# Kernel optimization log

Measured on AMD Instinct MI355X. Metric: run time of the kernel, lower is better.

The kernel has to match this reference:

```python
import jax, jax.numpy as jnp
import numpy as np

M, IN, OUT = 32, 4096, 16384

def setup_inputs() -> dict:
    key = jax.random.key(0)
    k1, k2, k3 = jax.random.split(key, 3)
    x = jax.random.normal(k1, (M, IN), dtype=jnp.float32)
    weight_q = jax.random.randint(k2, (OUT, IN), 0, 256, dtype=jnp.int32)  # uint8 codes
    bias = jax.random.normal(k3, (OUT,), dtype=jnp.float32)
    return {"x": x, "weight_q": weight_q, "zero": 128, "scale": jnp.float32(0.01), "bias": bias}

def reference(x, weight_q, zero, scale, bias):
    # Dequantize: w = scale * (q - zero), per-tensor affine
    w = scale * (weight_q.astype(jnp.float32) - jnp.float32(zero))  # [OUT, IN]
    # F.linear: y = x @ w.T + b
    return jnp.einsum('mi,oi->mo', x, w) + bias
```

## Files before the change

kernel.cpp:

```cpp
#include <hip/hip_runtime.h>

#define M_DIM 32
#define K_DIM 4096
#define N_DIM 16384
#define BN 16
#define BK 128
#define NSTAGE 32
#define LROW 136

using short8 = __attribute__((ext_vector_type(8))) short;
using f32x4  = __attribute__((ext_vector_type(4))) float;

__device__ __forceinline__ ushort f2bf_rne(float f) {
    unsigned u = __float_as_uint(f);
    u += 0x7fffu + ((u >> 16) & 1u);
    return (ushort)(u >> 16);
}

__device__ __forceinline__ ushort i2bf_exact(int v) {
    return (ushort)(__float_as_uint((float)v) >> 16);
}

__device__ __forceinline__ ushort4 cvt4(int4 v, int zero) {
    ushort4 o;
    o.x = i2bf_exact(v.x - zero);
    o.y = i2bf_exact(v.y - zero);
    o.z = i2bf_exact(v.z - zero);
    o.w = i2bf_exact(v.w - zero);
    return o;
}

__global__ __launch_bounds__(256) void prep_x_kernel(const float* __restrict__ x,
                                                     ushort* __restrict__ xb) {
    int i = blockIdx.x * blockDim.x + threadIdx.x;
    float4 v = reinterpret_cast<const float4*>(x)[i];
    ushort4 o;
    o.x = f2bf_rne(v.x); o.y = f2bf_rne(v.y); o.z = f2bf_rne(v.z); o.w = f2bf_rne(v.w);
    reinterpret_cast<ushort4*>(xb)[i] = o;
}

__global__ __launch_bounds__(256) void qgemm_kernel(
        const ushort* __restrict__ xb, const int* __restrict__ wq,
        const int* __restrict__ zerop, const float* __restrict__ scalep,
        const float* __restrict__ bias, float* __restrict__ out) {
    __shared__ ushort tile[BN][LROW];
    __shared__ float  red[4][M_DIM][BN];

    const int tid  = threadIdx.x;
    const int wave = tid >> 6;
    const int lane = tid & 63;
    const int quad = lane >> 4;
    const int l16  = lane & 15;
    const int n0   = blockIdx.x * BN;
    const int zero = *zerop;
    const int phase = blockIdx.x & (NSTAGE - 1);

    const int srow0 = wave * 4 + (lane >> 5);
    const int srow1 = srow0 + 2;
    const int sofs  = (lane & 31) * 4;
    const int* gb0 = wq + (size_t)(n0 + srow0) * K_DIM + sofs;
    const int* gb1 = wq + (size_t)(n0 + srow1) * K_DIM + sofs;

    const int bofs = wave * 32 + quad * 8;
    const ushort* axp0 = xb + (size_t)l16 * K_DIM + bofs;
    const ushort* axp1 = axp0 + 16 * K_DIM;

    f32x4 acc0 = {0.f, 0.f, 0.f, 0.f};
    f32x4 acc1 = {0.f, 0.f, 0.f, 0.f};

    int4 c0 = *(const int4*)(gb0 + phase * BK);
    int4 c1 = *(const int4*)(gb1 + phase * BK);

    #pragma unroll 1
    for (int s = 0; s < NSTAGE; ++s) {
        int4 nx0, nx1;
        if (s + 1 < NSTAGE) {
            int sn = ((s + 1 + phase) & (NSTAGE - 1)) * BK;
            nx0 = *(const int4*)(gb0 + sn);
            nx1 = *(const int4*)(gb1 + sn);
        }
        __syncthreads();
        *(ushort4*)&tile[srow0][sofs] = cvt4(c0, zero);
        *(ushort4*)&tile[srow1][sofs] = cvt4(c1, zero);
        __syncthreads();

        const int k0 = ((s + phase) & (NSTAGE - 1)) * BK;
        short8 a0 = *(const short8*)(axp0 + k0);
        short8 a1 = *(const short8*)(axp1 + k0);
        short8 bf = *(const short8*)&tile[l16][bofs];
        acc0 = __builtin_amdgcn_mfma_f32_16x16x32_bf16(a0, bf, acc0, 0, 0, 0);
        acc1 = __builtin_amdgcn_mfma_f32_16x16x32_bf16(a1, bf, acc1, 0, 0, 0);

        c0 = nx0; c1 = nx1;
    }

    __syncthreads();
    #pragma unroll
    for (int i = 0; i < 4; ++i) {
        red[wave][(quad << 2) + i][l16]      = acc0[i];
        red[wave][16 + (quad << 2) + i][l16] = acc1[i];
    }
    __syncthreads();

    const float scale = *scalep;
    #pragma unroll
    for (int t = 0; t < 2; ++t) {
        int idx = tid + (t << 8);
        int row = idx >> 4;
        int c   = idx & 15;
        float s = red[0][row][c] + red[1][row][c] + red[2][row][c] + red[3][row][c];
        out[(size_t)row * N_DIM + n0 + c] = fmaf(scale, s, bias[n0 + c]);
    }
}

extern "C" void kernel_launch(void* const* d_in, const int* in_sizes, int n_in,
                              void* d_out, int out_size, void* d_ws, size_t ws_size,
                              hipStream_t stream) {
    const float* x      = (const float*)d_in[0];
    const int*   wq     = (const int*)d_in[1];
    const int*   zerop  = (const int*)d_in[2];
    const float* scalep = (const float*)d_in[3];
    const float* bias   = (const float*)d_in[4];
    float*       out    = (float*)d_out;
    ushort*      xb     = (ushort*)d_ws;

    prep_x_kernel<<<(M_DIM * K_DIM / 4) / 256, 256, 0, stream>>>(x, xb);
    qgemm_kernel<<<N_DIM / BN, 256, 0, stream>>>(xb, wq, zerop, scalep, bias, out);
}
```

Baseline: 359.9 us.

## Split K across waves with per-wave LDS tiles and 32-column blocks

Each block now covers 32 output columns instead of 16, and each of the four waves owns a contiguous quarter of K with its own double-buffered LDS tile. This removes the two block-wide barriers per stage and replaces them with a per-wave lgkmcnt wait. Each wave issues four MFMAs per stage, so every loaded A fragment is reused across two column tiles. The grid is halved to 512 blocks, which lowers occupancy, and the global weight loads become 32-int row segments rather than 128-int segments, giving less contiguous access per row.

Result: slower. 378.4 us (+5.1%).

```diff
diff --git a/kernel.cpp b/kernel.cpp
--- a/kernel.cpp
+++ b/kernel.cpp
@@ -3,10 +3,9 @@
 #define M_DIM 32
 #define K_DIM 4096
 #define N_DIM 16384
-#define BN 16
-#define BK 128
-#define NSTAGE 32
-#define LROW 136
+#define WR  32
+#define NST 32
+#define LP  40
 
 using short8 = __attribute__((ext_vector_type(8))) short;
 using f32x4  = __attribute__((ext_vector_type(4))) float;
@@ -43,73 +42,85 @@
         const ushort* __restrict__ xb, const int* __restrict__ wq,
         const int* __restrict__ zerop, const float* __restrict__ scalep,
         const float* __restrict__ bias, float* __restrict__ out) {
-    __shared__ ushort tile[BN][LROW];
-    __shared__ float  red[4][M_DIM][BN];
+    __shared__ ushort wt[4][2][WR][LP];
+    __shared__ float  red[4][M_DIM][WR];
 
     const int tid  = threadIdx.x;
     const int wave = tid >> 6;
     const int lane = tid & 63;
     const int quad = lane >> 4;
     const int l16  = lane & 15;
-    const int n0   = blockIdx.x * BN;
+    const int n0   = blockIdx.x * WR;
     const int zero = *zerop;
-    const int phase = blockIdx.x & (NSTAGE - 1);
+    const int phase = blockIdx.x & (NST - 1);
+    const int kw   = wave << 10;
 
-    const int srow0 = wave * 4 + (lane >> 5);
-    const int srow1 = srow0 + 2;
-    const int sofs  = (lane & 31) * 4;
-    const int* gb0 = wq + (size_t)(n0 + srow0) * K_DIM + sofs;
-    const int* gb1 = wq + (size_t)(n0 + srow1) * K_DIM + sofs;
+    const int srow = lane >> 3;
+    const int scol = (lane & 7) << 2;
+    const int* gB  = wq + (size_t)(n0 + srow) * K_DIM + kw + scol;
 
-    const int bofs = wave * 32 + quad * 8;
-    const ushort* axp0 = xb + (size_t)l16 * K_DIM + bofs;
+    const ushort* axp0 = xb + (size_t)l16 * K_DIM + kw + (quad << 3);
     const ushort* axp1 = axp0 + 16 * K_DIM;
 
-    f32x4 acc0 = {0.f, 0.f, 0.f, 0.f};
-    f32x4 acc1 = {0.f, 0.f, 0.f, 0.f};
+    f32x4 c00 = {0.f,0.f,0.f,0.f}, c01 = {0.f,0.f,0.f,0.f};
+    f32x4 c10 = {0.f,0.f,0.f,0.f}, c11 = {0.f,0.f,0.f,0.f};
 
-    int4 c0 = *(const int4*)(gb0 + phase * BK);
-    int4 c1 = *(const int4*)(gb1 + phase * BK);
+    int sn0 = (phase & (NST - 1)) << 5;
+    int4 pb0 = *(const int4*)(gB +     sn0);
+    int4 pb1 = *(const int4*)(gB + 32768 + sn0);
+    int4 pb2 = *(const int4*)(gB + 65536 + sn0);
+    int4 pb3 = *(const int4*)(gB + 98304 + sn0);
+    short8 pa0 = *(const short8*)(axp0 + sn0);
+    short8 pa1 = *(const short8*)(axp1 + sn0);
 
-    #pragma unroll 1
-    for (int s = 0; s < NSTAGE; ++s) {
-        int4 nx0, nx1;
-        if (s + 1 < NSTAGE) {
-            int sn = ((s + 1 + phase) & (NSTAGE - 1)) * BK;
-            nx0 = *(const int4*)(gb0 + sn);
-            nx1 = *(const int4*)(gb1 + sn);
+    #pragma unroll 2
+    for (int s = 0; s < NST; ++s) {
+        int4 b0i = pb0, b1i = pb1, b2i = pb2, b3i = pb3;
+        short8 a0 = pa0, a1 = pa1;
+        if (s + 1 < NST) {
+            int sn = ((s + 1 + phase) & (NST - 1)) << 5;
+            pb0 = *(const int4*)(gB +         sn);
+            pb1 = *(const int4*)(gB + 32768 + sn);
+            pb2 = *(const int4*)(gB + 65536 + sn);
+            pb3 = *(const int4*)(gB + 98304 + sn);
+            pa0 = *(const short8*)(axp0 + sn);
+            pa1 = *(const short8*)(axp1 + sn);
         }
-        __syncthreads();
-        *(ushort4*)&tile[srow0][sofs] = cvt4(c0, zero);
-        *(ushort4*)&tile[srow1][sofs] = cvt4(c1, zero);
-        __syncthreads();
 
-        const int k0 = ((s + phase) & (NSTAGE - 1)) * BK;
-        short8 a0 = *(const short8*)(axp0 + k0);
-        short8 a1 = *(const short8*)(axp1 + k0);
-        short8 bf = *(const short8*)&tile[l16][bofs];
-        acc0 = __builtin_amdgcn_mfma_f32_16x16x32_bf16(a0, bf, acc0, 0, 0, 0);
-        acc1 = __builtin_amdgcn_mfma_f32_16x16x32_bf16(a1, bf, acc1, 0, 0, 0);
+        ushort* wp = &wt[wave][s & 1][srow][scol];
+        *(ushort4*)(wp)           = cvt4(b0i, zero);
+        *(ushort4*)(wp +  8 * LP) = cvt4(b1i, zero);
+        *(ushort4*)(wp + 16 * LP) = cvt4(b2i, zero);
+        *(ushort4*)(wp + 24 * LP) = cvt4(b3i, zero);
+        asm volatile("s_waitcnt lgkmcnt(0)" ::: "memory");
 
-        c0 = nx0; c1 = nx1;
+        const ushort* rp = &wt[wave][s & 1][l16][quad << 3];
+        short8 bf0 = *(const short8*)(rp);
+        short8 bf1 = *(const short8*)(rp + 16 * LP);
+        c00 = __builtin_amdgcn_mfma_f32_16x16x32_bf16(a0, bf0, c00, 0, 0, 0);
+        c01 = __builtin_amdgcn_mfma_f32_16x16x32_bf16(a0, bf1, c01, 0, 0, 0);
+        c10 = __builtin_amdgcn_mfma_f32_16x16x32_bf16(a1, bf0, c10, 0, 0, 0);
+        c11 = __builtin_amdgcn_mfma_f32_16x16x32_bf16(a1, bf1, c11, 0, 0, 0);
     }
 
-    __syncthreads();
     #pragma unroll
     for (int i = 0; i < 4; ++i) {
-        red[wave][(quad << 2) + i][l16]      = acc0[i];
-        red[wave][16 + (quad << 2) + i][l16] = acc1[i];
+        red[wave][(quad << 2) + i     ][l16     ] = c00[i];
+        red[wave][(quad << 2) + i     ][l16 + 16] = c01[i];
+        red[wave][(quad << 2) + i + 16][l16     ] = c10[i];
+        red[wave][(quad << 2) + i + 16][l16 + 16] = c11[i];
     }
     __syncthreads();
 
     const float scale = *scalep;
     #pragma unroll
-    for (int t = 0; t < 2; ++t) {
+    for (int t = 0; t < 4; ++t) {
         int idx = tid + (t << 8);
-        int row = idx >> 4;
-        int c   = idx & 15;
-        float s = red[0][row][c] + red[1][row][c] + red[2][row][c] + red[3][row][c];
-        out[(size_t)row * N_DIM + n0 + c] = fmaf(scale, s, bias[n0 + c]);
+        int row = idx >> 5;
+        int col = idx & 31;
+        float s = red[0][row][col] + red[1][row][col]
+                + red[2][row][col] + red[3][row][col];
+        out[(size_t)row * N_DIM + n0 + col] = fmaf(scale, s, bias[n0 + col]);
     }
 }
 
@@ -125,5 +136,5 @@
     ushort*      xb     = (ushort*)d_ws;
 
     prep_x_kernel<<<(M_DIM * K_DIM / 4) / 256, 256, 0, stream>>>(x, xb);
-    qgemm_kernel<<<N_DIM / BN, 256, 0, stream>>>(xb, wq, zerop, scalep, bias, out);
+    qgemm_kernel<<<N_DIM / WR, 256, 0, stream>>>(xb, wq, zerop, scalep, bias, out);
 }
```

## Deepen weight prefetch to two stages and prefetch activations with LDS-only barriers

Applied to the files above, without the earlier changes.

Weight loads are issued two iterations ahead instead of one, and the bf16 activation fragments are prefetched one iteration ahead rather than loaded just before the MFMAs. __syncthreads is replaced by an inline-asm barrier that waits only on lgkmcnt, so outstanding global loads (vmcnt) are not drained at each barrier. The loop is unrolled by 2. This targets the exposed global memory latency in this memory-bound loop, at the cost of more live registers. The custom barrier depends on the compiler not inserting its own vmcnt waits.

Measured after the change: 361.3 us. Within noise of the previous version (+0.4%).

```diff
diff --git a/kernel.cpp b/kernel.cpp
--- a/kernel.cpp
+++ b/kernel.cpp
@@ -10,6 +10,8 @@
 
 using short8 = __attribute__((ext_vector_type(8))) short;
 using f32x4  = __attribute__((ext_vector_type(4))) float;
+
+#define LDS_BARRIER() asm volatile("s_waitcnt lgkmcnt(0)\n\ts_barrier" ::: "memory")
 
 __device__ __forceinline__ ushort f2bf_rne(float f) {
     unsigned u = __float_as_uint(f);
@@ -68,30 +70,42 @@
     f32x4 acc0 = {0.f, 0.f, 0.f, 0.f};
     f32x4 acc1 = {0.f, 0.f, 0.f, 0.f};
 
-    int4 c0 = *(const int4*)(gb0 + phase * BK);
-    int4 c1 = *(const int4*)(gb1 + phase * BK);
+    const int k0p = phase * BK;
+    const int k1p = ((1 + phase) & (NSTAGE - 1)) * BK;
+    int4 c0 = *(const int4*)(gb0 + k0p);
+    int4 c1 = *(const int4*)(gb1 + k0p);
+    int4 d0 = *(const int4*)(gb0 + k1p);
+    int4 d1 = *(const int4*)(gb1 + k1p);
+    short8 a0c = *(const short8*)(axp0 + k0p);
+    short8 a1c = *(const short8*)(axp1 + k0p);
 
-    #pragma unroll 1
+    #pragma unroll 2
     for (int s = 0; s < NSTAGE; ++s) {
-        int4 nx0, nx1;
+        int4 nb0, nb1;
+        if (s + 2 < NSTAGE) {
+            int sn = ((s + 2 + phase) & (NSTAGE - 1)) * BK;
+            nb0 = *(const int4*)(gb0 + sn);
+            nb1 = *(const int4*)(gb1 + sn);
+        }
+        short8 na0, na1;
         if (s + 1 < NSTAGE) {
-            int sn = ((s + 1 + phase) & (NSTAGE - 1)) * BK;
-            nx0 = *(const int4*)(gb0 + sn);
-            nx1 = *(const int4*)(gb1 + sn);
+            int ka = ((s + 1 + phase) & (NSTAGE - 1)) * BK;
+            na0 = *(const short8*)(axp0 + ka);
+            na1 = *(const short8*)(axp1 + ka);
         }
-        __syncthreads();
+
+        LDS_BARRIER();
         *(ushort4*)&tile[srow0][sofs] = cvt4(c0, zero);
         *(ushort4*)&tile[srow1][sofs] = cvt4(c1, zero);
-        __syncthreads();
+        LDS_BARRIER();
 
-        const int k0 = ((s + phase) & (NSTAGE - 1)) * BK;
-        short8 a0 = *(const short8*)(axp0 + k0);
-        short8 a1 = *(const short8*)(axp1 + k0);
         short8 bf = *(const short8*)&tile[l16][bofs];
-        acc0 = __builtin_amdgcn_mfma_f32_16x16x32_bf16(a0, bf, acc0, 0, 0, 0);
-        acc1 = __builtin_amdgcn_mfma_f32_16x16x32_bf16(a1, bf, acc1, 0, 0, 0);
+        acc0 = __builtin_amdgcn_mfma_f32_16x16x32_bf16(a0c, bf, acc0, 0, 0, 0);
+        acc1 = __builtin_amdgcn_mfma_f32_16x16x32_bf16(a1c, bf, acc1, 0, 0, 0);
 
-        c0 = nx0; c1 = nx1;
+        c0 = d0; c1 = d1;
+        d0 = nb0; d1 = nb1;
+        a0c = na0; a1c = na1;
     }
 
     __syncthreads();
```

## Split K across blocks with partial sums and a separate reduce kernel

Applied to the files above, without the earlier changes.

Replaces the single-pass kernel, which looped over all of K per 16-column tile with double-buffered staging, with a split-K scheme. Each block takes a quarter of K, loads its whole 16x1024 weight slab into LDS at once, and converts x to bf16 inline instead of in a separate prep kernel. Partial results go to a workspace buffer, and a second kernel sums the four partials and applies scale and bias. This gives four times as many blocks and far fewer barriers, which should help hide latency on the weight stream. The cost is extra partial-sum traffic of 8 MB written and read back, redundant x conversion in every block, and a larger LDS footprint per block.

After: 383.9 us. 1.07x slower.

```diff
diff --git a/kernel.cpp b/kernel.cpp
--- a/kernel.cpp
+++ b/kernel.cpp
@@ -3,10 +3,8 @@
 #define M_DIM 32
 #define K_DIM 4096
 #define N_DIM 16384
-#define BN 16
-#define BK 128
-#define NSTAGE 32
-#define LROW 136
+#define KQ 1024
+#define LP 1032
 
 using short8 = __attribute__((ext_vector_type(8))) short;
 using f32x4  = __attribute__((ext_vector_type(4))) float;
@@ -30,71 +28,58 @@
     return o;
 }
 
-__global__ __launch_bounds__(256) void prep_x_kernel(const float* __restrict__ x,
-                                                     ushort* __restrict__ xb) {
-    int i = blockIdx.x * blockDim.x + threadIdx.x;
-    float4 v = reinterpret_cast<const float4*>(x)[i];
-    ushort4 o;
-    o.x = f2bf_rne(v.x); o.y = f2bf_rne(v.y); o.z = f2bf_rne(v.z); o.w = f2bf_rne(v.w);
-    reinterpret_cast<ushort4*>(xb)[i] = o;
-}
-
-__global__ __launch_bounds__(256) void qgemm_kernel(
-        const ushort* __restrict__ xb, const int* __restrict__ wq,
-        const int* __restrict__ zerop, const float* __restrict__ scalep,
-        const float* __restrict__ bias, float* __restrict__ out) {
-    __shared__ ushort tile[BN][LROW];
-    __shared__ float  red[4][M_DIM][BN];
+__global__ __launch_bounds__(256) void qgemm_part_kernel(
+        const float* __restrict__ x, const int* __restrict__ wq,
+        const int* __restrict__ zerop, float* __restrict__ partial) {
+    __shared__ ushort tile[16][LP];
+    __shared__ float  red[4][M_DIM][16];
 
     const int tid  = threadIdx.x;
     const int wave = tid >> 6;
     const int lane = tid & 63;
     const int quad = lane >> 4;
     const int l16  = lane & 15;
-    const int n0   = blockIdx.x * BN;
+    const int kq   = blockIdx.x & 3;
+    const int nt   = blockIdx.x >> 2;
+    const int n0   = nt << 4;
+    const int kbase = kq << 10;
     const int zero = *zerop;
-    const int phase = blockIdx.x & (NSTAGE - 1);
 
-    const int srow0 = wave * 4 + (lane >> 5);
-    const int srow1 = srow0 + 2;
-    const int sofs  = (lane & 31) * 4;
-    const int* gb0 = wq + (size_t)(n0 + srow0) * K_DIM + sofs;
-    const int* gb1 = wq + (size_t)(n0 + srow1) * K_DIM + sofs;
-
-    const int bofs = wave * 32 + quad * 8;
-    const ushort* axp0 = xb + (size_t)l16 * K_DIM + bofs;
-    const ushort* axp1 = axp0 + 16 * K_DIM;
+    const int* gW = wq + (size_t)n0 * K_DIM + kbase;
+    #pragma unroll
+    for (int i = 0; i < 16; ++i) {
+        int4 v = *(const int4*)(gW + ((size_t)i << 12) + (tid << 2));
+        *(ushort4*)&tile[i][tid << 2] = cvt4(v, zero);
+    }
+    __syncthreads();
 
     f32x4 acc0 = {0.f, 0.f, 0.f, 0.f};
     f32x4 acc1 = {0.f, 0.f, 0.f, 0.f};
+    const int kl0 = wave << 8;
+    const float* ax0 = x + (size_t)l16 * K_DIM + kbase + kl0 + (quad << 3);
+    const float* ax1 = ax0 + 16 * K_DIM;
 
-    int4 c0 = *(const int4*)(gb0 + phase * BK);
-    int4 c1 = *(const int4*)(gb1 + phase * BK);
-
-    #pragma unroll 1
-    for (int s = 0; s < NSTAGE; ++s) {
-        int4 nx0, nx1;
-        if (s + 1 < NSTAGE) {
-            int sn = ((s + 1 + phase) & (NSTAGE - 1)) * BK;
-            nx0 = *(const int4*)(gb0 + sn);
-            nx1 = *(const int4*)(gb1 + sn);
-        }
-        __syncthreads();
-        *(ushort4*)&tile[srow0][sofs] = cvt4(c0, zero);
-        *(ushort4*)&tile[srow1][sofs] = cvt4(c1, zero);
-        __syncthreads();
-
-        const int k0 = ((s + phase) & (NSTAGE - 1)) * BK;
-        short8 a0 = *(const short8*)(axp0 + k0);
-        short8 a1 = *(const short8*)(axp1 + k0);
-        short8 bf = *(const short8*)&tile[l16][bofs];
+    #pragma unroll
+    for (int s = 0; s < 8; ++s) {
+        const int ko = s << 5;
+        float4 lo0 = *(const float4*)(ax0 + ko);
+        float4 hi0 = *(const float4*)(ax0 + ko + 4);
+        float4 lo1 = *(const float4*)(ax1 + ko);
+        float4 hi1 = *(const float4*)(ax1 + ko + 4);
+        short8 a0, a1;
+        a0[0] = (short)f2bf_rne(lo0.x); a0[1] = (short)f2bf_rne(lo0.y);
+        a0[2] = (short)f2bf_rne(lo0.z); a0[3] = (short)f2bf_rne(lo0.w);
+        a0[4] = (short)f2bf_rne(hi0.x); a0[5] = (short)f2bf_rne(hi0.y);
+        a0[6] = (short)f2bf_rne(hi0.z); a0[7] = (short)f2bf_rne(hi0.w);
+        a1[0] = (short)f2bf_rne(lo1.x); a1[1] = (short)f2bf_rne(lo1.y);
+        a1[2] = (short)f2bf_rne(lo1.z); a1[3] = (short)f2bf_rne(lo1.w);
+        a1[4] = (short)f2bf_rne(hi1.x); a1[5] = (short)f2bf_rne(hi1.y);
+        a1[6] = (short)f2bf_rne(hi1.z); a1[7] = (short)f2bf_rne(hi1.w);
+        short8 bf = *(const short8*)&tile[l16][kl0 + ko + (quad << 3)];
         acc0 = __builtin_amdgcn_mfma_f32_16x16x32_bf16(a0, bf, acc0, 0, 0, 0);
         acc1 = __builtin_amdgcn_mfma_f32_16x16x32_bf16(a1, bf, acc1, 0, 0, 0);
-
-        c0 = nx0; c1 = nx1;
     }
 
-    __syncthreads();
     #pragma unroll
     for (int i = 0; i < 4; ++i) {
         red[wave][(quad << 2) + i][l16]      = acc0[i];
@@ -102,15 +87,31 @@
     }
     __syncthreads();
 
-    const float scale = *scalep;
     #pragma unroll
     for (int t = 0; t < 2; ++t) {
         int idx = tid + (t << 8);
         int row = idx >> 4;
-        int c   = idx & 15;
-        float s = red[0][row][c] + red[1][row][c] + red[2][row][c] + red[3][row][c];
-        out[(size_t)row * N_DIM + n0 + c] = fmaf(scale, s, bias[n0 + c]);
+        int col = idx & 15;
+        float s = red[0][row][col] + red[1][row][col]
+                + red[2][row][col] + red[3][row][col];
+        partial[(size_t)(kq * M_DIM + row) * N_DIM + n0 + col] = s;
     }
+}
+
+__global__ __launch_bounds__(256) void reduce_kernel(
+        const float* __restrict__ partial, const float* __restrict__ scalep,
+        const float* __restrict__ bias, float* __restrict__ out) {
+    const int j = blockIdx.x * 256 + threadIdx.x;
+    const float4* p = (const float4*)partial;
+    float4 p0 = p[j], p1 = p[j + 131072], p2 = p[j + 262144], p3 = p[j + 393216];
+    const float sc = *scalep;
+    float4 b4 = *(const float4*)(bias + ((j & 4095) << 2));
+    float4 o;
+    o.x = fmaf(sc, p0.x + p1.x + p2.x + p3.x, b4.x);
+    o.y = fmaf(sc, p0.y + p1.y + p2.y + p3.y, b4.y);
+    o.z = fmaf(sc, p0.z + p1.z + p2.z + p3.z, b4.z);
+    o.w = fmaf(sc, p0.w + p1.w + p2.w + p3.w, b4.w);
+    ((float4*)out)[j] = o;
 }
 
 extern "C" void kernel_launch(void* const* d_in, const int* in_sizes, int n_in,
@@ -122,8 +123,8 @@
     const float* scalep = (const float*)d_in[3];
     const float* bias   = (const float*)d_in[4];
     float*       out    = (float*)d_out;
-    ushort*      xb     = (ushort*)d_ws;
+    float*       part   = (float*)d_ws;
 
-    prep_x_kernel<<<(M_DIM * K_DIM / 4) / 256, 256, 0, stream>>>(x, xb);
-    qgemm_kernel<<<N_DIM / BN, 256, 0, stream>>>(xb, wq, zerop, scalep, bias, out);
+    qgemm_part_kernel<<<4096, 256, 0, stream>>>(x, wq, zerop, part);
+    reduce_kernel<<<512, 256, 0, stream>>>(part, scalep, bias, out);
 }
```
